# Optimization experiments

Hardware: AMD Instinct MI355X
Metric: run time of the kernel (lower is better)

The kernel has to match this reference:

```python
import jax, jax.numpy as jnp
import numpy as np
from jax import lax


def _lstm(x, W_ih, W_hh, b_ih, b_hh, return_seq):
    """PyTorch-compatible single-layer LSTM, batch_first, zero init state.
    W_ih: [4H, D], W_hh: [4H, H], gate order (i, f, g, o).
    Returns [B, T, H] if return_seq else final hidden [B, H]."""
    B, T, _ = x.shape
    H = W_hh.shape[1]
    # Precompute input contribution for all timesteps: [B, T, 4H]
    xg = jnp.einsum('btd,gd->btg', x, W_ih) + b_ih + b_hh
    h0 = jnp.zeros((B, H), x.dtype)
    c0 = jnp.zeros((B, H), x.dtype)

    def step(carry, xt):
        h, c = carry
        g = xt + h @ W_hh.T  # [B, 4H]
        i, f, gg, o = jnp.split(g, 4, axis=-1)
        i = jax.nn.sigmoid(i)
        f = jax.nn.sigmoid(f)
        gg = jnp.tanh(gg)
        o = jax.nn.sigmoid(o)
        c = f * c + i * gg
        h = o * jnp.tanh(c)
        return (h, c), (h if return_seq else None)

    (hT, _), ys = lax.scan(step, (h0, c0), jnp.swapaxes(xg, 0, 1))
    if return_seq:
        return jnp.swapaxes(ys, 0, 1)  # [B, T, H]
    return hT


def setup_inputs() -> dict:
    key = jax.random.key(0)
    ks = jax.random.split(key, 12)
    B, T, D = 2048, 512, 64
    H1, H2 = 16, 4
    s = 0.1
    return {
        'x': jax.random.normal(ks[0], (B, T, D), jnp.float32),
        'W_ih1': jax.random.normal(ks[1], (4 * H1, D), jnp.float32) * s,
        'W_hh1': jax.random.normal(ks[2], (4 * H1, H1), jnp.float32) * s,
        'b_ih1': jax.random.normal(ks[3], (4 * H1,), jnp.float32) * s,
        'b_hh1': jax.random.normal(ks[4], (4 * H1,), jnp.float32) * s,
        'W_ih2': jax.random.normal(ks[5], (4 * H2, H1), jnp.float32) * s,
        'W_hh2': jax.random.normal(ks[6], (4 * H2, H2), jnp.float32) * s,
        'b_ih2': jax.random.normal(ks[7], (4 * H2,), jnp.float32) * s,
        'b_hh2': jax.random.normal(ks[8], (4 * H2,), jnp.float32) * s,
        'W_fc': jax.random.normal(ks[9], (D, H2), jnp.float32) * s,
        'b_fc': jax.random.normal(ks[10], (D,), jnp.float32) * s,
    }


def reference(x, W_ih1, W_hh1, b_ih1, b_hh1, W_ih2, W_hh2, b_ih2, b_hh2, W_fc, b_fc):
    y = _lstm(x, W_ih1, W_hh1, b_ih1, b_hh1, return_seq=True)  # [B, T, H1]
    y = jax.nn.relu(y)
    # Only the last timestep of lstm2 is used -> return final hidden state.
    y_last = _lstm(y, W_ih2, W_hh2, b_ih2, b_hh2, return_seq=False)  # [B, H2]
    out = y_last @ W_fc.T + b_fc  # [B, D]
    return jax.nn.sigmoid(out)
```

## Files before the change

kernel.cpp:

```cpp
#include <hip/hip_runtime.h>
#include <hip/hip_bf16.h>

#define T_ALL 512
#define TB 16
#define NB (T_ALL / TB)
#define LOG2E 1.44269504088896f

typedef __attribute__((ext_vector_type(8))) short bf16x8;
typedef __attribute__((ext_vector_type(4))) float f32x4;

#define DPPF(v, CTRL) __uint_as_float((unsigned)__builtin_amdgcn_update_dpp(0, (int)__float_as_uint(v), (CTRL), 0xF, 0xF, true))
#define SWZF(v, PAT)  __uint_as_float((unsigned)__builtin_amdgcn_ds_swizzle((int)__float_as_uint(v), (PAT)))
#define BPERM(a, v)   __uint_as_float((unsigned)__builtin_amdgcn_ds_bpermute((a), (int)__float_as_uint(v)))

__device__ __forceinline__ unsigned pack2bf16(float a, float b) {
    unsigned ua = __float_as_uint(a), ub = __float_as_uint(b);
    ua += 0x7FFFu + ((ua >> 16) & 1u);
    ub += 0x7FFFu + ((ub >> 16) & 1u);
    return (ua >> 16) | (ub & 0xFFFF0000u);
}
__device__ __forceinline__ bf16x8 make_frag(float4 lo, float4 hi) {
    union { unsigned u[4]; bf16x8 v; } r;
    r.u[0] = pack2bf16(lo.x, lo.y);
    r.u[1] = pack2bf16(lo.z, lo.w);
    r.u[2] = pack2bf16(hi.x, hi.y);
    r.u[3] = pack2bf16(hi.z, hi.w);
    return r.v;
}
__device__ __forceinline__ float4 scale4(float4 v, float s) {
    return make_float4(v.x * s, v.y * s, v.z * s, v.w * s);
}
__device__ __forceinline__ float2 pkfma(float2 a, float2 b, float2 c) {
    return make_float2(fmaf(a.x, b.x, c.x), fmaf(a.y, b.y, c.y));
}
__device__ __forceinline__ float fsigm(float x) {
    return __builtin_amdgcn_rcpf(1.0f + __builtin_amdgcn_exp2f(-LOG2E * x));
}

__global__ __launch_bounds__(64, 2)
void lstm_fused_v5(const float* __restrict__ x,
        const float* __restrict__ Wih1, const float* __restrict__ Whh1,
        const float* __restrict__ bih1, const float* __restrict__ bhh1,
        const float* __restrict__ Wih2, const float* __restrict__ Whh2,
        const float* __restrict__ bih2, const float* __restrict__ bhh2,
        const float* __restrict__ Wfc,  const float* __restrict__ bfc,
        float* __restrict__ out)
{
    __shared__ __align__(16) float xg[TB * 64];

    const int lane = threadIdx.x;
    const int tl = lane & 15;
    const int kh = lane >> 4;
    const size_t b = blockIdx.x;

    const int T1 = lane & 3;
    const int j1 = lane >> 2;
    const int m2 = lane >> 4;
    const int T2 = (lane >> 2) & 3;

    const float aA1 = (T1 == 2) ? 2.0f : 1.0f, aB1 = (T1 == 2) ? -1.0f : 0.0f;
    const float aA2 = (T2 == 2) ? 2.0f : 1.0f, aB2 = (T2 == 2) ? -1.0f : 0.0f;
    const float sc2 = (T2 == 2) ? 2.0f * LOG2E : LOG2E;

    bf16x8 wb[4][2];
    float bias1[4];
#pragma unroll
    for (int n = 0; n < 4; ++n) {
        const float scn = (n == 2) ? 2.0f * LOG2E : LOG2E;
#pragma unroll
        for (int kk = 0; kk < 2; ++kk) {
            const float* wp = Wih1 + (size_t)(n * 16 + tl) * 64 + kk * 32 + kh * 8;
            wb[n][kk] = make_frag(scale4(*(const float4*)wp, scn),
                                  scale4(*(const float4*)(wp + 4), scn));
        }
        bias1[n] = (bih1[n * 16 + tl] + bhh1[n * 16 + tl]) * scn;
    }

    float2 wq01[4], wq23[4];
    {
        const float sA = (T1 == 2) ? 2.0f * LOG2E : LOG2E;
        const float sB = ((T1 ^ 2) == 2) ? 2.0f * LOG2E : LOG2E;
        const float sC = ((T1 ^ 1) == 2) ? 2.0f * LOG2E : LOG2E;
        const float sD = ((T1 ^ 3) == 2) ? 2.0f * LOG2E : LOG2E;
        const float4 wa = scale4(*(const float4*)(Whh1 + (T1 * 16 + j1) * 16 + 4 * T1), sA);
        const float4 wbv = scale4(*(const float4*)(Whh1 + ((T1 ^ 2) * 16 + j1) * 16 + 4 * T1), sB);
        const float4 wc = scale4(*(const float4*)(Whh1 + ((T1 ^ 1) * 16 + j1) * 16 + 4 * T1), sC);
        const float4 wd = scale4(*(const float4*)(Whh1 + ((T1 ^ 3) * 16 + j1) * 16 + 4 * T1), sD);
        wq01[0] = make_float2(wa.x, wbv.x); wq23[0] = make_float2(wc.x, wd.x);
        wq01[1] = make_float2(wa.y, wbv.y); wq23[1] = make_float2(wc.y, wd.y);
        wq01[2] = make_float2(wa.z, wbv.z); wq23[2] = make_float2(wc.z, wd.z);
        wq01[3] = make_float2(wa.w, wbv.w); wq23[3] = make_float2(wc.w, wd.w);
    }

    const int row2 = T2 * 4 + m2;
    const float4 w2q = scale4(*(const float4*)(Wih2 + row2 * 16 + 4 * T1), sc2);
    const float2 w2a = make_float2(w2q.x, w2q.y);
    const float2 w2b = make_float2(w2q.z, w2q.w);
    const float w2h = Whh2[row2 * 4 + T1] * sc2;
    const float bias2l = (T1 == 0) ? (bih2[row2] + bhh2[row2]) * sc2 : 0.0f;

    const float4 wfc = *(const float4*)(Wfc + lane * 4);
    const float bfcv = bfc[lane];

    int ga[4];
#pragma unroll
    for (int u = 0; u < 4; ++u)
        ga[u] = (16 * T1 + 4 * u + kh) << 2;
    const int ha2 = T1 << 6;
    const int xoff = (T1 * 16 + j1) << 2;

    float c1 = 0.f, h1 = 0.f, c2 = 0.f, h2v = 0.f, h2s = 0.f;
    float g0 = 0.f, g1 = 0.f, g2 = 0.f, g3 = 0.f;

    const float* xb = x + b * (size_t)(T_ALL * 64);

    float4 xpf[4];
#pragma unroll
    for (int kk = 0; kk < 2; ++kk)
#pragma unroll
        for (int hf = 0; hf < 2; ++hf)
            xpf[kk * 2 + hf] = *(const float4*)(xb + tl * 64 + kk * 32 + kh * 8 + hf * 4);

    for (int c = 0; c < NB; ++c) {
        bf16x8 a0 = make_frag(xpf[0], xpf[1]);
        bf16x8 a1 = make_frag(xpf[2], xpf[3]);
        if (c + 1 < NB) {
            const float* src = xb + (size_t)(c + 1) * (TB * 64);
#pragma unroll
            for (int kk = 0; kk < 2; ++kk)
#pragma unroll
                for (int hf = 0; hf < 2; ++hf)
                    xpf[kk * 2 + hf] = *(const float4*)(src + tl * 64 + kk * 32 + kh * 8 + hf * 4);
        }

#pragma unroll
        for (int n = 0; n < 4; ++n) {
            f32x4 acc = {bias1[n], bias1[n], bias1[n], bias1[n]};
            acc = __builtin_amdgcn_mfma_f32_16x16x32_bf16(a0, wb[n][0], acc, 0, 0, 0);
            acc = __builtin_amdgcn_mfma_f32_16x16x32_bf16(a1, wb[n][1], acc, 0, 0, 0);
#pragma unroll
            for (int r = 0; r < 4; ++r)
                xg[(kh * 4 + r) * 64 + n * 16 + tl] = acc[r];
        }

#pragma unroll
        for (int tt = 0; tt < TB; ++tt) {
            const float xu = *(const float*)((const char*)xg + (tt * 256) + xoff);

            {
                const float r0 = fmaxf(g0, 0.f), r1 = fmaxf(g1, 0.f);
                const float r2 = fmaxf(g2, 0.f), r3 = fmaxf(g3, 0.f);
                float2 a2 = make_float2(bias2l, w2h * h2s);
                a2 = pkfma(w2a, make_float2(r0, r1), a2);
                a2 = pkfma(w2b, make_float2(r2, r3), a2);
                float p2 = a2.x + a2.y;
                p2 += DPPF(p2, 0xB1);
                p2 += DPPF(p2, 0x4E);
                const float act2 = fmaf(aA2,
                    __builtin_amdgcn_rcpf(1.0f + __builtin_amdgcn_exp2f(-p2)), aB2);
                const float fv2 = SWZF(act2, 0x101F);
                const float gv2 = SWZF(act2, 0x201F);
                const float ov2 = SWZF(act2, 0x301F);
                const float c2n = fmaf(fv2, c2, act2 * gv2);
                const float ec2 = __builtin_amdgcn_exp2f(-2.0f * LOG2E * c2n);
                const float h2n = ov2 * fmaf(2.0f, __builtin_amdgcn_rcpf(1.0f + ec2), -1.0f);
                if ((c | tt) != 0) { c2 = c2n; h2v = h2n; }
                h2s = BPERM(ha2, h2v);
            }

            float2 acc01 = make_float2(0.f, 0.f), acc23 = make_float2(0.f, 0.f);
            acc01 = pkfma(wq01[0], make_float2(g0, g0), acc01);
            acc23 = pkfma(wq23[0], make_float2(g0, g0), acc23);
            acc01 = pkfma(wq01[1], make_float2(g1, g1), acc01);
            acc23 = pkfma(wq23[1], make_float2(g1, g1), acc23);
            acc01 = pkfma(wq01[2], make_float2(g2, g2), acc01);
            acc23 = pkfma(wq23[2], make_float2(g2, g2), acc23);
            acc01 = pkfma(wq01[3], make_float2(g3, g3), acc01);
            acc23 = pkfma(wq23[3], make_float2(g3, g3), acc23);
            const float q0 = acc01.x + DPPF(acc23.x, 0xB1);
            const float q1 = acc01.y + DPPF(acc23.y, 0xB1);
            const float pre = q0 + DPPF(q1, 0x4E) + xu;

            const float act = fmaf(aA1,
                __builtin_amdgcn_rcpf(1.0f + __builtin_amdgcn_exp2f(-pre)), aB1);
            const float iv = DPPF(act, 0x00);
            const float fv = DPPF(act, 0x55);
            const float gv = DPPF(act, 0xAA);
            const float ov = DPPF(act, 0xFF);
            c1 = fmaf(fv, c1, iv * gv);
            const float ec = __builtin_amdgcn_exp2f(-2.0f * LOG2E * c1);
            h1 = ov * fmaf(2.0f, __builtin_amdgcn_rcpf(1.0f + ec), -1.0f);

            g0 = BPERM(ga[0], h1);
            g1 = BPERM(ga[1], h1);
            g2 = BPERM(ga[2], h1);
            g3 = BPERM(ga[3], h1);
        }
    }

    {
        const float r0 = fmaxf(g0, 0.f), r1 = fmaxf(g1, 0.f);
        const float r2 = fmaxf(g2, 0.f), r3 = fmaxf(g3, 0.f);
        float2 a2 = make_float2(bias2l, w2h * h2s);
        a2 = pkfma(w2a, make_float2(r0, r1), a2);
        a2 = pkfma(w2b, make_float2(r2, r3), a2);
        float p2 = a2.x + a2.y;
        p2 += DPPF(p2, 0xB1);
        p2 += DPPF(p2, 0x4E);
        const float act2 = fmaf(aA2,
            __builtin_amdgcn_rcpf(1.0f + __builtin_amdgcn_exp2f(-p2)), aB2);
        const float fv2 = SWZF(act2, 0x101F);
        const float gv2 = SWZF(act2, 0x201F);
        const float ov2 = SWZF(act2, 0x301F);
        c2 = fmaf(fv2, c2, act2 * gv2);
        const float ec2 = __builtin_amdgcn_exp2f(-2.0f * LOG2E * c2);
        h2v = ov2 * fmaf(2.0f, __builtin_amdgcn_rcpf(1.0f + ec2), -1.0f);
    }

    const float hq0 = __shfl(h2v, 0);
    const float hq1 = __shfl(h2v, 16);
    const float hq2 = __shfl(h2v, 32);
    const float hq3 = __shfl(h2v, 48);
    float accf = bfcv;
    accf = fmaf(wfc.x, hq0, accf);
    accf = fmaf(wfc.y, hq1, accf);
    accf = fmaf(wfc.z, hq2, accf);
    accf = fmaf(wfc.w, hq3, accf);
    out[b * 64 + lane] = fsigm(accf);
}

extern "C" void kernel_launch(void* const* d_in, const int* in_sizes, int n_in,
                              void* d_out, int out_size, void* d_ws, size_t ws_size,
                              hipStream_t stream) {
    const float* x    = (const float*)d_in[0];
    const float* Wih1 = (const float*)d_in[1];
    const float* Whh1 = (const float*)d_in[2];
    const float* bih1 = (const float*)d_in[3];
    const float* bhh1 = (const float*)d_in[4];
    const float* Wih2 = (const float*)d_in[5];
    const float* Whh2 = (const float*)d_in[6];
    const float* bih2 = (const float*)d_in[7];
    const float* bhh2 = (const float*)d_in[8];
    const float* Wfc  = (const float*)d_in[9];
    const float* bfc  = (const float*)d_in[10];
    float* out = (float*)d_out;

    lstm_fused_v5<<<dim3(2048), dim3(64), 0, stream>>>(
        x, Wih1, Whh1, bih1, bhh1, Wih2, Whh2, bih2, bhh2, Wfc, bfc, out);
}
```

Measured before the change: 171.6 us.

## Restructure LSTM step to overlap layer-1 tanh with layer-2 gate activation

Reworks the per-timestep recurrence so one exp/rcp pass serves two purposes: lanes 0-15 evaluate tanh of the layer-1 cell state while the other lanes evaluate the layer-2 gate activations. The layer-1 cell and output gate are broadcast with bpermute, and layer-2 preactivations are pipelined one step behind. This shortens the serial dependency chain per step and removes separate transcendental passes. It also pads the shared xg buffer to a stride of 68 to avoid bank conflicts, and regroups the W_hh multiply into per-gate packed FMAs. The cost is extra bpermutes and more complex lane-role logic, which is harder to verify.

```diff
diff --git a/kernel.cpp b/kernel.cpp
--- a/kernel.cpp
+++ b/kernel.cpp
@@ -5,12 +5,12 @@
 #define TB 16
 #define NB (T_ALL / TB)
 #define LOG2E 1.44269504088896f
+#define XSTR 68
 
 typedef __attribute__((ext_vector_type(8))) short bf16x8;
 typedef __attribute__((ext_vector_type(4))) float f32x4;
 
 #define DPPF(v, CTRL) __uint_as_float((unsigned)__builtin_amdgcn_update_dpp(0, (int)__float_as_uint(v), (CTRL), 0xF, 0xF, true))
-#define SWZF(v, PAT)  __uint_as_float((unsigned)__builtin_amdgcn_ds_swizzle((int)__float_as_uint(v), (PAT)))
 #define BPERM(a, v)   __uint_as_float((unsigned)__builtin_amdgcn_ds_bpermute((a), (int)__float_as_uint(v)))
 
 __device__ __forceinline__ unsigned pack2bf16(float a, float b) {
@@ -33,12 +33,16 @@
 __device__ __forceinline__ float2 pkfma(float2 a, float2 b, float2 c) {
     return make_float2(fmaf(a.x, b.x, c.x), fmaf(a.y, b.y, c.y));
 }
+__device__ __forceinline__ float tanh_c(float c) {
+    return fmaf(2.0f, __builtin_amdgcn_rcpf(
+        1.0f + __builtin_amdgcn_exp2f(-2.0f * LOG2E * c)), -1.0f);
+}
 __device__ __forceinline__ float fsigm(float x) {
     return __builtin_amdgcn_rcpf(1.0f + __builtin_amdgcn_exp2f(-LOG2E * x));
 }
 
 __global__ __launch_bounds__(64, 2)
-void lstm_fused_v5(const float* __restrict__ x,
+void lstm_fused_v7(const float* __restrict__ x,
         const float* __restrict__ Wih1, const float* __restrict__ Whh1,
         const float* __restrict__ bih1, const float* __restrict__ bhh1,
         const float* __restrict__ Wih2, const float* __restrict__ Whh2,
@@ -46,7 +50,7 @@
         const float* __restrict__ Wfc,  const float* __restrict__ bfc,
         float* __restrict__ out)
 {
-    __shared__ __align__(16) float xg[TB * 64];
+    __shared__ __align__(16) float xs[TB * XSTR];
 
     const int lane = threadIdx.x;
     const int tl = lane & 15;
@@ -55,12 +59,12 @@
 
     const int T1 = lane & 3;
     const int j1 = lane >> 2;
-    const int m2 = lane >> 4;
-    const int T2 = (lane >> 2) & 3;
 
     const float aA1 = (T1 == 2) ? 2.0f : 1.0f, aB1 = (T1 == 2) ? -1.0f : 0.0f;
-    const float aA2 = (T2 == 2) ? 2.0f : 1.0f, aB2 = (T2 == 2) ? -1.0f : 0.0f;
-    const float sc2 = (T2 == 2) ? 2.0f * LOG2E : LOG2E;
+    const bool lo16 = (lane < 16);
+    const float esc = lo16 ? (-2.0f * LOG2E) : -1.0f;
+    const bool bt = lo16 || ((lane & 3) == 2);
+    const float aAb = bt ? 2.0f : 1.0f, aBb = bt ? -1.0f : 0.0f;
 
     bf16x8 wb[4][2];
     float bias1[4];
@@ -76,23 +80,26 @@
         bias1[n] = (bih1[n * 16 + tl] + bhh1[n * 16 + tl]) * scn;
     }
 
-    float2 wq01[4], wq23[4];
+    float2 wrA0, wrA1, wrB0, wrB1, wrC0, wrC1, wrD0, wrD1;
     {
         const float sA = (T1 == 2) ? 2.0f * LOG2E : LOG2E;
         const float sB = ((T1 ^ 2) == 2) ? 2.0f * LOG2E : LOG2E;
         const float sC = ((T1 ^ 1) == 2) ? 2.0f * LOG2E : LOG2E;
         const float sD = ((T1 ^ 3) == 2) ? 2.0f * LOG2E : LOG2E;
-        const float4 wa = scale4(*(const float4*)(Whh1 + (T1 * 16 + j1) * 16 + 4 * T1), sA);
+        const float4 wa  = scale4(*(const float4*)(Whh1 + ((T1    ) * 16 + j1) * 16 + 4 * T1), sA);
         const float4 wbv = scale4(*(const float4*)(Whh1 + ((T1 ^ 2) * 16 + j1) * 16 + 4 * T1), sB);
-        const float4 wc = scale4(*(const float4*)(Whh1 + ((T1 ^ 1) * 16 + j1) * 16 + 4 * T1), sC);
-        const float4 wd = scale4(*(const float4*)(Whh1 + ((T1 ^ 3) * 16 + j1) * 16 + 4 * T1), sD);
-        wq01[0] = make_float2(wa.x, wbv.x); wq23[0] = make_float2(wc.x, wd.x);
-        wq01[1] = make_float2(wa.y, wbv.y); wq23[1] = make_float2(wc.y, wd.y);
-        wq01[2] = make_float2(wa.z, wbv.z); wq23[2] = make_float2(wc.z, wd.z);
-        wq01[3] = make_float2(wa.w, wbv.w); wq23[3] = make_float2(wc.w, wd.w);
-    }
-
+        const float4 wc  = scale4(*(const float4*)(Whh1 + ((T1 ^ 1) * 16 + j1) * 16 + 4 * T1), sC);
+        const float4 wd  = scale4(*(const float4*)(Whh1 + ((T1 ^ 3) * 16 + j1) * 16 + 4 * T1), sD);
+        wrA0 = make_float2(wa.x, wa.y);   wrA1 = make_float2(wa.z, wa.w);
+        wrB0 = make_float2(wbv.x, wbv.y); wrB1 = make_float2(wbv.z, wbv.w);
+        wrC0 = make_float2(wc.x, wc.y);   wrC1 = make_float2(wc.z, wc.w);
+        wrD0 = make_float2(wd.x, wd.y);   wrD1 = make_float2(wd.z, wd.w);
+    }
+
+    const int m2 = lane >> 4;
+    const int T2 = (lane >> 2) & 3;
     const int row2 = T2 * 4 + m2;
+    const float sc2 = (T2 == 2) ? 2.0f * LOG2E : LOG2E;
     const float4 w2q = scale4(*(const float4*)(Wih2 + row2 * 16 + 4 * T1), sc2);
     const float2 w2a = make_float2(w2q.x, w2q.y);
     const float2 w2b = make_float2(w2q.z, w2q.w);
@@ -102,15 +109,71 @@
     const float4 wfc = *(const float4*)(Wfc + lane * 4);
     const float bfcv = bfc[lane];
 
-    int ga[4];
-#pragma unroll
-    for (int u = 0; u < 4; ++u)
-        ga[u] = (16 * T1 + 4 * u + kh) << 2;
-    const int ha2 = T1 << 6;
-    const int xoff = (T1 * 16 + j1) << 2;
-
-    float c1 = 0.f, h1 = 0.f, c2 = 0.f, h2v = 0.f, h2s = 0.f;
-    float g0 = 0.f, g1 = 0.f, g2 = 0.f, g3 = 0.f;
+    const int ag0 = (4 * T1 + 0) << 2;
+    const int ag1 = (4 * T1 + 1) << 2;
+    const int ag2 = (4 * T1 + 2) << 2;
+    const int ag3 = (4 * T1 + 3) << 2;
+    const int ac1 = (4 * (lane & 15)) << 2;
+    const int ao1 = ((4 * (lane & 15)) + 3) << 2;
+    const int ah2 = (16 + 4 * (lane & 3)) << 2;
+    const int ap2 = (16 * ((lane >> 2) & 3) + 4 * (lane & 3)) << 2;
+
+    const int gidx = T1 * 16 + j1;
+
+    float c1r = 0.f;
+    float c1b = 0.f;
+    float o1b = 0.f;
+    float p2b = 0.f;
+    float c2q = 0.f;
+    float h2r = 0.f;
+
+#define STEP(XU) do { \
+    const float _vb = lo16 ? c1b : p2b; \
+    const float _e = __builtin_amdgcn_exp2f(esc * _vb); \
+    const float _sb = __builtin_amdgcn_rcpf(1.0f + _e); \
+    const float _outB = fmaf(aAb, _sb, aBb);             \
+    const float _h1 = o1b * _outB;                       \
+    const float _g0 = BPERM(ag0, _h1); \
+    const float _g1 = BPERM(ag1, _h1); \
+    const float _g2 = BPERM(ag2, _h1); \
+    const float _g3 = BPERM(ag3, _h1); \
+    const float2 _g01 = make_float2(_g0, _g1); \
+    const float2 _g23 = make_float2(_g2, _g3); \
+    float2 _aA = pkfma(wrA0, _g01, make_float2((XU), 0.f)); _aA = pkfma(wrA1, _g23, _aA); \
+    float2 _aB = pkfma(wrB0, _g01, make_float2(0.f, 0.f)); _aB = pkfma(wrB1, _g23, _aB); \
+    float2 _aC = pkfma(wrC0, _g01, make_float2(0.f, 0.f)); _aC = pkfma(wrC1, _g23, _aC); \
+    float2 _aD = pkfma(wrD0, _g01, make_float2(0.f, 0.f)); _aD = pkfma(wrD1, _g23, _aD); \
+    const float _sA = _aA.x + _aA.y, _sB2 = _aB.x + _aB.y; \
+    const float _sC = _aC.x + _aC.y, _sD = _aD.x + _aD.y; \
+    const float _u0 = _sA + DPPF(_sC, 0xB1); \
+    const float _u1 = _sB2 + DPPF(_sD, 0xB1); \
+    const float _pre = _u0 + DPPF(_u1, 0x4E); \
+    const float _s1 = __builtin_amdgcn_rcpf(1.0f + __builtin_amdgcn_exp2f(-_pre)); \
+    const float _act = fmaf(aA1, _s1, aB1);              \
+    const float _iv = DPPF(_act, 0x00); \
+    const float _fv = DPPF(_act, 0x55); \
+    const float _gv = DPPF(_act, 0xAA); \
+    c1r = fmaf(_fv, c1r, _iv * _gv);                     \
+    c1b = BPERM(ac1, c1r); \
+    o1b = BPERM(ao1, _act); \
+    { \
+        const float _i2 = DPPF(_outB, 0x00); \
+        const float _f2 = DPPF(_outB, 0x55); \
+        const float _g2v = DPPF(_outB, 0xAA); \
+        const float _o2 = DPPF(_outB, 0xFF); \
+        c2q = fmaf(_f2, c2q, _i2 * _g2v);                \
+        h2r = _o2 * tanh_c(c2q);                         \
+    } \
+    const float _h2s = BPERM(ah2, h2r); \
+    const float2 _r01 = make_float2(fmaxf(_g01.x, 0.f), fmaxf(_g01.y, 0.f)); \
+    const float2 _r23 = make_float2(fmaxf(_g23.x, 0.f), fmaxf(_g23.y, 0.f)); \
+    float2 _a2 = pkfma(w2a, _r01, make_float2(bias2l, w2h * _h2s)); \
+    _a2 = pkfma(w2b, _r23, _a2); \
+    float _p2 = _a2.x + _a2.y; \
+    _p2 += DPPF(_p2, 0xB1); \
+    _p2 += DPPF(_p2, 0x4E);                              \
+    p2b = BPERM(ap2, _p2); \
+} while (0)
 
     const float* xb = x + b * (size_t)(T_ALL * 64);
 
@@ -140,93 +203,47 @@
             acc = __builtin_amdgcn_mfma_f32_16x16x32_bf16(a1, wb[n][1], acc, 0, 0, 0);
 #pragma unroll
             for (int r = 0; r < 4; ++r)
-                xg[(kh * 4 + r) * 64 + n * 16 + tl] = acc[r];
-        }
-
-#pragma unroll
-        for (int tt = 0; tt < TB; ++tt) {
-            const float xu = *(const float*)((const char*)xg + (tt * 256) + xoff);
-
-            {
-                const float r0 = fmaxf(g0, 0.f), r1 = fmaxf(g1, 0.f);
-                const float r2 = fmaxf(g2, 0.f), r3 = fmaxf(g3, 0.f);
-                float2 a2 = make_float2(bias2l, w2h * h2s);
-                a2 = pkfma(w2a, make_float2(r0, r1), a2);
-                a2 = pkfma(w2b, make_float2(r2, r3), a2);
-                float p2 = a2.x + a2.y;
-                p2 += DPPF(p2, 0xB1);
-                p2 += DPPF(p2, 0x4E);
-                const float act2 = fmaf(aA2,
-                    __builtin_amdgcn_rcpf(1.0f + __builtin_amdgcn_exp2f(-p2)), aB2);
-                const float fv2 = SWZF(act2, 0x101F);
-                const float gv2 = SWZF(act2, 0x201F);
-                const float ov2 = SWZF(act2, 0x301F);
-                const float c2n = fmaf(fv2, c2, act2 * gv2);
-                const float ec2 = __builtin_amdgcn_exp2f(-2.0f * LOG2E * c2n);
-                const float h2n = ov2 * fmaf(2.0f, __builtin_amdgcn_rcpf(1.0f + ec2), -1.0f);
-                if ((c | tt) != 0) { c2 = c2n; h2v = h2n; }
-                h2s = BPERM(ha2, h2v);
-            }
-
-            float2 acc01 = make_float2(0.f, 0.f), acc23 = make_float2(0.f, 0.f);
-            acc01 = pkfma(wq01[0], make_float2(g0, g0), acc01);
-            acc23 = pkfma(wq23[0], make_float2(g0, g0), acc23);
-            acc01 = pkfma(wq01[1], make_float2(g1, g1), acc01);
-            acc23 = pkfma(wq23[1], make_float2(g1, g1), acc23);
-            acc01 = pkfma(wq01[2], make_float2(g2, g2), acc01);
-            acc23 = pkfma(wq23[2], make_float2(g2, g2), acc23);
-            acc01 = pkfma(wq01[3], make_float2(g3, g3), acc01);
-            acc23 = pkfma(wq23[3], make_float2(g3, g3), acc23);
-            const float q0 = acc01.x + DPPF(acc23.x, 0xB1);
-            const float q1 = acc01.y + DPPF(acc23.y, 0xB1);
-            const float pre = q0 + DPPF(q1, 0x4E) + xu;
-
-            const float act = fmaf(aA1,
-                __builtin_amdgcn_rcpf(1.0f + __builtin_amdgcn_exp2f(-pre)), aB1);
-            const float iv = DPPF(act, 0x00);
-            const float fv = DPPF(act, 0x55);
-            const float gv = DPPF(act, 0xAA);
-            const float ov = DPPF(act, 0xFF);
-            c1 = fmaf(fv, c1, iv * gv);
-            const float ec = __builtin_amdgcn_exp2f(-2.0f * LOG2E * c1);
-            h1 = ov * fmaf(2.0f, __builtin_amdgcn_rcpf(1.0f + ec), -1.0f);
-
-            g0 = BPERM(ga[0], h1);
-            g1 = BPERM(ga[1], h1);
-            g2 = BPERM(ga[2], h1);
-            g3 = BPERM(ga[3], h1);
-        }
-    }
+                xs[(kh * 4 + r) * XSTR + n * 16 + tl] = acc[r];
+        }
+
+        if (c == 0) {
+            STEP(xs[0 * XSTR + gidx]);
+            p2b = 0.f;
+#pragma unroll
+            for (int tt = 1; tt < TB; ++tt)
+                STEP(xs[tt * XSTR + gidx]);
+        } else {
+#pragma unroll
+            for (int tt = 0; tt < TB; ++tt)
+                STEP(xs[tt * XSTR + gidx]);
+        }
+    }
+
+    STEP(0.0f);
 
     {
-        const float r0 = fmaxf(g0, 0.f), r1 = fmaxf(g1, 0.f);
-        const float r2 = fmaxf(g2, 0.f), r3 = fmaxf(g3, 0.f);
-        float2 a2 = make_float2(bias2l, w2h * h2s);
-        a2 = pkfma(w2a, make_float2(r0, r1), a2);
-        a2 = pkfma(w2b, make_float2(r2, r3), a2);
-        float p2 = a2.x + a2.y;
-        p2 += DPPF(p2, 0xB1);
-        p2 += DPPF(p2, 0x4E);
-        const float act2 = fmaf(aA2,
-            __builtin_amdgcn_rcpf(1.0f + __builtin_amdgcn_exp2f(-p2)), aB2);
-        const float fv2 = SWZF(act2, 0x101F);
-        const float gv2 = SWZF(act2, 0x201F);
-        const float ov2 = SWZF(act2, 0x301F);
-        c2 = fmaf(fv2, c2, act2 * gv2);
-        const float ec2 = __builtin_amdgcn_exp2f(-2.0f * LOG2E * c2);
-        h2v = ov2 * fmaf(2.0f, __builtin_amdgcn_rcpf(1.0f + ec2), -1.0f);
-    }
-
-    const float hq0 = __shfl(h2v, 0);
-    const float hq1 = __shfl(h2v, 16);
-    const float hq2 = __shfl(h2v, 32);
-    const float hq3 = __shfl(h2v, 48);
-    float accf = bfcv;
-    accf = fmaf(wfc.x, hq0, accf);
-    accf = fmaf(wfc.y, hq1, accf);
-    accf = fmaf(wfc.z, hq2, accf);
-    accf = fmaf(wfc.w, hq3, accf);
-    out[b * 64 + lane] = fsigm(accf);
+        const float e2 = __builtin_amdgcn_exp2f(-p2b);
+        const float sb2 = __builtin_amdgcn_rcpf(1.0f + e2);
+        const float outB2 = fmaf(aAb, sb2, aBb);
+        const float i2 = DPPF(outB2, 0x00);
+        const float f2 = DPPF(outB2, 0x55);
+        const float g2v = DPPF(outB2, 0xAA);
+        const float o2 = DPPF(outB2, 0xFF);
+        c2q = fmaf(f2, c2q, i2 * g2v);
+        const float h2f = o2 * tanh_c(c2q);
+
+        const float hm0 = __shfl(h2f, 16);
+        const float hm1 = __shfl(h2f, 20);
+        const float hm2 = __shfl(h2f, 24);
+        const float hm3 = __shfl(h2f, 28);
+        float accf = bfcv;
+        accf = fmaf(wfc.x, hm0, accf);
+        accf = fmaf(wfc.y, hm1, accf);
+        accf = fmaf(wfc.z, hm2, accf);
+        accf = fmaf(wfc.w, hm3, accf);
+        out[b * 64 + lane] = fsigm(accf);
+    }
+#undef STEP
 }
 
 extern "C" void kernel_launch(void* const* d_in, const int* in_sizes, int n_in,
@@ -245,6 +262,6 @@
     const float* bfc  = (const float*)d_in[10];
     float* out = (float*)d_out;
 
-    lstm_fused_v5<<<dim3(2048), dim3(64), 0, stream>>>(
+    lstm_fused_v7<<<dim3(2048), dim3(64), 0, stream>>>(
         x, Wih1, Whh1, bih1, bhh1, Wih2, Whh2, bih2, bhh2, Wfc, bfc, out);
 }
```

New measurement: 190.2 us. +10.9%, slower.
